# Kernel tuning notes

Hardware: AMD Instinct MI355X
Metric: run time of the kernel (lower is better)

Reference implementation:

```python
import jax, jax.numpy as jnp
from jax import lax
import numpy as np

C = 256       # residual_channels == skip_channels
B = 4
T = 4096
LATENT = 128
NB = 4        # n_blocks
NL = 10       # n_layers
ENC_DILS = tuple(2 ** i for i in range(NL)) * NB   # 40 encoder blocks
DEC_DILS = tuple(2 ** i for i in range(NL))        # 10 decoder blocks


def causal_conv(x, W, b, d):
    # x: [B, Cin, T], W: [Cout, Cin, k], left-pad by (k-1)*d for causality
    pad = (W.shape[-1] - 1) * d
    y = lax.conv_general_dilated(x, W, (1,), [(pad, 0)], rhs_dilation=(d,),
                                 dimension_numbers=('NCH', 'OIH', 'NCH'))
    return y + b[None, :, None]


def gated_block(h, Wf, bf, Wg, bg, Wr, br, Ws, bs, d):
    f = jnp.tanh(causal_conv(h, Wf, bf, d))
    g = jax.nn.sigmoid(causal_conv(h, Wg, bg, d))
    out = f * g
    res = jnp.einsum('oc,bct->bot', Wr, out) + br[None, :, None] + h
    skip = jnp.einsum('oc,bct->bot', Ws, out) + bs[None, :, None]
    return res, skip


def setup_inputs() -> dict:
    key = jax.random.key(0)
    ks = jax.random.split(key, 24)
    s = 0.05
    nE = NB * NL
    d = {}
    d['x'] = jax.random.normal(ks[0], (B, 1, T), jnp.float32)
    d['eps'] = jax.random.normal(ks[1], (B, LATENT), jnp.float32)
    d['enc_in_W'] = jax.random.normal(ks[2], (C, 1, 2)) * s
    d['enc_in_b'] = jnp.zeros((C,), jnp.float32)
    d['enc_Wf'] = jax.random.normal(ks[3], (nE, C, C, 2)) * s
    d['enc_bf'] = jnp.zeros((nE, C), jnp.float32)
    d['enc_Wg'] = jax.random.normal(ks[4], (nE, C, C, 2)) * s
    d['enc_bg'] = jnp.zeros((nE, C), jnp.float32)
    d['enc_Wr'] = jax.random.normal(ks[5], (nE, C, C)) * s
    d['enc_br'] = jnp.zeros((nE, C), jnp.float32)
    d['enc_Ws'] = jax.random.normal(ks[6], (nE, C, C)) * s
    d['enc_bs'] = jnp.zeros((nE, C), jnp.float32)
    d['fc_mu_W'] = jax.random.normal(ks[7], (LATENT, C)) * s
    d['fc_mu_b'] = jnp.zeros((LATENT,), jnp.float32)
    d['fc_lv_W'] = jax.random.normal(ks[8], (LATENT, C)) * s
    d['fc_lv_b'] = jnp.zeros((LATENT,), jnp.float32)
    d['dec_in_W'] = jax.random.normal(ks[9], (C, LATENT)) * s
    d['dec_in_b'] = jnp.zeros((C,), jnp.float32)
    d['dec_Wf'] = jax.random.normal(ks[10], (NL, C, C, 2)) * s
    d['dec_bf'] = jnp.zeros((NL, C), jnp.float32)
    d['dec_Wg'] = jax.random.normal(ks[11], (NL, C, C, 2)) * s
    d['dec_bg'] = jnp.zeros((NL, C), jnp.float32)
    d['dec_Wr'] = jax.random.normal(ks[12], (NL, C, C)) * s
    d['dec_br'] = jnp.zeros((NL, C), jnp.float32)
    d['out_W'] = jax.random.normal(ks[13], (1, C)) * s
    d['out_b'] = jnp.zeros((1,), jnp.float32)
    return d


def _forward(x, eps, enc_in_W, enc_in_b, enc_Wf, enc_bf, enc_Wg, enc_bg,
             enc_Wr, enc_br, enc_Ws, enc_bs, fc_mu_W, fc_mu_b, fc_lv_W, fc_lv_b,
             dec_in_W, dec_in_b, dec_Wf, dec_bf, dec_Wg, dec_bg, dec_Wr, dec_br,
             out_W, out_b):
    # --- encode ---
    h = causal_conv(x, enc_in_W, enc_in_b, 1)
    skip_sum = jnp.zeros((h.shape[0], C, h.shape[2]), h.dtype)
    for i, dil in enumerate(ENC_DILS):
        h, skip = gated_block(h, enc_Wf[i], enc_bf[i], enc_Wg[i], enc_bg[i],
                              enc_Wr[i], enc_br[i], enc_Ws[i], enc_bs[i], dil)
        skip_sum = skip_sum + skip
    pooled = skip_sum.mean(axis=-1)                      # [B, C]
    mu = pooled @ fc_mu_W.T + fc_mu_b                    # [B, LATENT]
    logvar = pooled @ fc_lv_W.T + fc_lv_b
    # --- reparameterize ---
    z = mu + eps * jnp.exp(0.5 * logvar)
    # --- decode (length-1 sequence) ---
    h2 = (jnp.einsum('ol,bl->bo', dec_in_W, z) + dec_in_b)[:, :, None]  # [B, C, 1]
    for i, dil in enumerate(DEC_DILS):
        f = jnp.tanh(causal_conv(h2, dec_Wf[i], dec_bf[i], dil))
        g = jax.nn.sigmoid(causal_conv(h2, dec_Wg[i], dec_bg[i], dil))
        out = f * g
        h2 = jnp.einsum('oc,bct->bot', dec_Wr[i], out) + dec_br[i][None, :, None] + h2
    y = jnp.einsum('oc,bct->bot', out_W, h2) + out_b[None, :, None]     # [B, 1, 1]
    return (y, mu, logvar)


def reference(x, eps, enc_in_W, enc_in_b, enc_Wf, enc_bf, enc_Wg, enc_bg,
              enc_Wr, enc_br, enc_Ws, enc_bs, fc_mu_W, fc_mu_b, fc_lv_W, fc_lv_b,
              dec_in_W, dec_in_b, dec_Wf, dec_bf, dec_Wg, dec_bg, dec_Wr, dec_br,
              out_W, out_b):
    return _forward(x, eps, enc_in_W, enc_in_b, enc_Wf, enc_bf, enc_Wg, enc_bg,
                    enc_Wr, enc_br, enc_Ws, enc_bs, fc_mu_W, fc_mu_b, fc_lv_W, fc_lv_b,
                    dec_in_W, dec_in_b, dec_Wf, dec_bf, dec_Wg, dec_bg, dec_Wr, dec_br,
                    out_W, out_b)
```

## Files before the change

### kernel.cpp

```cpp
#include <hip/hip_runtime.h>

typedef unsigned short u16;
typedef __attribute__((ext_vector_type(8))) __bf16 bf16x8;
typedef __attribute__((ext_vector_type(4))) float f32x4;

constexpr int C = 256;
constexpr int T = 4096;
constexpr int B = 4;
constexpr int NENC = 40;
constexpr int NDEC = 10;
constexpr int TILE = 64;

__device__ __forceinline__ float bf2f(u16 v) {
  union { unsigned u; float f; } x;
  x.u = ((unsigned)v) << 16;
  return x.f;
}
__device__ __forceinline__ u16 f2bf(float f) {
  union { float ff; unsigned u; } x;
  x.ff = f;
  unsigned r = x.u + 0x7fffu + ((x.u >> 16) & 1u);
  return (u16)(r >> 16);
}
__device__ __forceinline__ int swz(int row, int col) {
  int g = ((row & 7) ^ (row >> 3)) & 7;
  return row * 512 + (col ^ (g << 3));
}

typedef __attribute__((address_space(1))) const unsigned int* gp1_t;
typedef __attribute__((address_space(3))) unsigned int* lp3_t;
__device__ __forceinline__ void gl_lds16(const u16* g, u16* l) {
  __builtin_amdgcn_global_load_lds((gp1_t)(const void*)g, (lp3_t)(void*)l, 16, 0, 0);
}

__global__ void k_pack1(const float* __restrict__ Wf, const float* __restrict__ Wg,
                        u16* __restrict__ penc1, int total) {
  int p = blockIdx.x * 256 + threadIdx.x;
  if (p >= total) return;
  int lane = p & 63;
  int s = (p >> 6) & 3;
  int c = (p >> 8) & 15;
  int wv = (p >> 12) & 7;
  int layer = p >> 15;
  int co = wv * 32 + (s & 1) * 16 + (lane & 15);
  int k = c * 32 + (lane >> 4) * 8;
  const float* src = (s >= 2 ? Wg : Wf) + ((size_t)layer * C + co) * 512 + k;
  u16* dst = penc1 + (size_t)p * 8;
#pragma unroll
  for (int r = 0; r < 8; ++r) dst[r] = f2bf(src[r]);
}

__global__ void k_pack2(const float* __restrict__ Wr, u16* __restrict__ penc2, int total) {
  int p = blockIdx.x * 256 + threadIdx.x;
  if (p >= total) return;
  int lane = p & 63;
  int s = (p >> 6) & 1;
  int c = (p >> 7) & 7;
  int wv = (p >> 10) & 7;
  int layer = p >> 13;
  int co = wv * 32 + s * 16 + (lane & 15);
  int k = c * 32 + (lane >> 4) * 8;
  const float* src = Wr + ((size_t)layer * C + co) * 256 + k;
  u16* dst = penc2 + (size_t)p * 8;
#pragma unroll
  for (int r = 0; r < 8; ++r) dst[r] = f2bf(src[r]);
}

__global__ void k_packd(const float* __restrict__ dWf, const float* __restrict__ dWg,
                        const float* __restrict__ dWr, const float* __restrict__ dinW,
                        u16* __restrict__ pdfg, u16* __restrict__ pdr,
                        u16* __restrict__ tdin) {
  int p = blockIdx.x * 256 + threadIdx.x;
  if (p < 163840) {
    int lane = p & 63;
    int s = (p >> 6) & 1;
    int c = (p >> 7) & 7;
    int wv = (p >> 10) & 15;
    int layer = p >> 14;
    int co = wv * 16 + (lane & 15);
    int k = c * 32 + (lane >> 4) * 8;
    const float* src = (s ? dWg : dWf) + (((size_t)(layer * C + co)) * C + k) * 2 + 1;
    u16* dst = pdfg + (size_t)p * 8;
#pragma unroll
    for (int r = 0; r < 8; ++r) dst[r] = f2bf(src[2 * r]);
  } else if (p < 245760) {
    int q = p - 163840;
    int lane = q & 63;
    int c = (q >> 6) & 7;
    int wv = (q >> 9) & 15;
    int layer = q >> 13;
    int co = wv * 16 + (lane & 15);
    int k = c * 32 + (lane >> 4) * 8;
    const float* src = dWr + ((size_t)(layer * C + co)) * C + k;
    u16* dst = pdr + (size_t)q * 8;
#pragma unroll
    for (int r = 0; r < 8; ++r) dst[r] = f2bf(src[r]);
  } else if (p < 249856) {
    int u = p - 245760;
#pragma unroll
    for (int r = 0; r < 8; ++r) tdin[u * 8 + r] = f2bf(dinW[u * 8 + r]);
  }
}

__global__ void k_zero(float* __restrict__ p, int n) {
  int i = blockIdx.x * 256 + threadIdx.x;
  if (i < n) p[i] = 0.f;
}

__global__ void k_input(const float* __restrict__ x, const float* __restrict__ W,
                        const float* __restrict__ bin, float* __restrict__ h) {
  int idx = blockIdx.x * 256 + threadIdx.x;
  int t = idx & (T - 1);
  int c = (idx >> 12) & (C - 1);
  int b = idx >> 20;
  float xv = x[b * T + t];
  float xp = (t > 0) ? x[b * T + t - 1] : 0.f;
  h[idx] = W[2 * c] * xp + W[2 * c + 1] * xv + bin[c];
}

__global__ __launch_bounds__(512, 2) void k_enc(
    const float* __restrict__ hin, float* __restrict__ hout, float* __restrict__ rowsum_l,
    const u16* __restrict__ pw1, const float* __restrict__ bfb,
    const float* __restrict__ bgb,
    const u16* __restrict__ pw2, const float* __restrict__ brb,
    int dil) {
  extern __shared__ __align__(16) u16 smem[];
  u16* wb = smem + 64 * 512;
  const int tid = threadIdx.x;
  const int wave = tid >> 6;
  const int lane = tid & 63;
  const int ncol = lane & 15;
  const int quad = lane >> 4;
  const int wg = blockIdx.x;
  const int b = wg >> 6;
  const int t0 = (wg & 63) * TILE;
  const float* hb = hin + b * C * T;

  const int co0 = wave * 32;
  const int kq = quad * 8;
  const u16* b1 = pw1 + wave * 32768 + lane * 8;
  const u16* b2 = pw2 + wave * 8192 + lane * 8;
  const int aoff = lane * 8;

#pragma unroll
  for (int q = 0; q < 3; ++q) {
    u16* ld = wb + q * 16384 + wave * 2048;
    const u16* gs = b1 + q * 2048;
    gl_lds16(gs, ld);
    gl_lds16(gs + 512, ld + 512);
    gl_lds16(gs + 1024, ld + 1024);
    gl_lds16(gs + 1536, ld + 1536);
  }

  const int n4 = tid & 15;
  const int cib = tid >> 4;
  float4 v[16];
  const bool al4 = ((dil & 3) == 0);
  if (t0 >= dil) {
#pragma unroll
    for (int it2 = 0; it2 < 16; ++it2) {
      int ci = (cib + it2 * 32) & 255;
      int tap = it2 >> 3;
      int tb = t0 + n4 * 4 - (tap ? 0 : dil);
      const float* p = hb + ci * T + tb;
      if (tap || al4) {
        v[it2] = *(const float4*)p;
      } else {
        v[it2].x = p[0]; v[it2].y = p[1]; v[it2].z = p[2]; v[it2].w = p[3];
      }
    }
  } else {
#pragma unroll
    for (int it2 = 0; it2 < 16; ++it2) {
      int ci = (cib + it2 * 32) & 255;
      int tap = it2 >> 3;
      int tb = t0 + n4 * 4 - (tap ? 0 : dil);
      const float* p = hb + ci * T + tb;
      if (tap) {
        v[it2] = *(const float4*)p;
      } else {
        v[it2].x = (tb + 0 >= 0) ? p[0] : 0.f;
        v[it2].y = (tb + 1 >= 0) ? p[1] : 0.f;
        v[it2].z = (tb + 2 >= 0) ? p[2] : 0.f;
        v[it2].w = (tb + 3 >= 0) ? p[3] : 0.f;
      }
    }
  }
#pragma unroll
  for (int it2 = 0; it2 < 8; ++it2) {
    int ci = (cib + it2 * 32) & 255;
    const float* p0 = (const float*)&v[it2];
    const float* p1 = (const float*)&v[it2 + 8];
#pragma unroll
    for (int r = 0; r < 4; ++r) {
      unsigned w32 = (unsigned)f2bf(p0[r]) | ((unsigned)f2bf(p1[r]) << 16);
      *(unsigned*)(&smem[swz(n4 * 4 + r, 2 * ci)]) = w32;
    }
  }
  __syncthreads();

  f32x4 acc[4][4];
#pragma unroll
  for (int m = 0; m < 4; ++m)
#pragma unroll
    for (int nt = 0; nt < 4; ++nt)
      acc[m][nt] = (f32x4){0.f, 0.f, 0.f, 0.f};

#pragma unroll
  for (int c = 0; c < 16; ++c) {
    if (c <= 13)      asm volatile("s_waitcnt vmcnt(8)" ::: "memory");
    else if (c == 14) asm volatile("s_waitcnt vmcnt(4)" ::: "memory");
    else              asm volatile("s_waitcnt vmcnt(0)" ::: "memory");
    const u16* wr_ = wb + (c % 3) * 16384 + wave * 2048;
    bf16x8 af0 = *(const bf16x8*)(wr_ + aoff);
    bf16x8 af1 = *(const bf16x8*)(wr_ + 512 + aoff);
    bf16x8 af2 = *(const bf16x8*)(wr_ + 1024 + aoff);
    bf16x8 af3 = *(const bf16x8*)(wr_ + 1536 + aoff);
    const int kk = c * 32 + kq;
    bf16x8 bfr[4];
#pragma unroll
    for (int nt = 0; nt < 4; ++nt)
      bfr[nt] = *(const bf16x8*)(&smem[swz(nt * 16 + ncol, kk)]);
#pragma unroll
    for (int nt = 0; nt < 4; ++nt) {
      acc[0][nt] = __builtin_amdgcn_mfma_f32_16x16x32_bf16(af0, bfr[nt], acc[0][nt], 0, 0, 0);
      acc[1][nt] = __builtin_amdgcn_mfma_f32_16x16x32_bf16(af1, bfr[nt], acc[1][nt], 0, 0, 0);
      acc[2][nt] = __builtin_amdgcn_mfma_f32_16x16x32_bf16(af2, bfr[nt], acc[2][nt], 0, 0, 0);
      acc[3][nt] = __builtin_amdgcn_mfma_f32_16x16x32_bf16(af3, bfr[nt], acc[3][nt], 0, 0, 0);
    }
    if (c + 3 < 16) {
      asm volatile("s_waitcnt lgkmcnt(0)" ::: "memory");
      u16* ld = wb + (c % 3) * 16384 + wave * 2048;
      const u16* gs = b1 + (c + 3) * 2048;
      gl_lds16(gs, ld);
      gl_lds16(gs + 512, ld + 512);
      gl_lds16(gs + 1024, ld + 1024);
      gl_lds16(gs + 1536, ld + 1536);
    }
  }

#pragma unroll
  for (int q = 0; q < 3; ++q) {
    u16* ld = wb + q * 16384 + wave * 2048;
    const u16* gs = b2 + q * 1024;
    gl_lds16(gs, ld);
    gl_lds16(gs + 512, ld + 512);
  }
  __syncthreads();

  float* rsb = rowsum_l + b * C;
#pragma unroll
  for (int j = 0; j < 2; ++j) {
    const int cob = co0 + j * 16 + quad * 4;
    float bfv[4], bgv[4], rs[4];
#pragma unroll
    for (int r = 0; r < 4; ++r) {
      bfv[r] = bfb[cob + r];
      bgv[r] = bgb[cob + r];
      rs[r] = 0.f;
    }
#pragma unroll
    for (int nt = 0; nt < 4; ++nt) {
      const int n = nt * 16 + ncol;
      u16 pk[4];
#pragma unroll
      for (int r = 0; r < 4; ++r) {
        float fv = acc[j][nt][r] + bfv[r];
        float gv = acc[2 + j][nt][r] + bgv[r];
        float th = 1.f - 2.f / (__expf(2.f * fv) + 1.f);
        float sg = 1.f / (1.f + __expf(-gv));
        float o = th * sg;
        rs[r] += o;
        pk[r] = f2bf(o);
      }
      uint2 w;
      w.x = (unsigned)pk[0] | ((unsigned)pk[1] << 16);
      w.y = (unsigned)pk[2] | ((unsigned)pk[3] << 16);
      *(uint2*)(&smem[swz(n, cob)]) = w;
    }
#pragma unroll
    for (int r = 0; r < 4; ++r) {
      float s = rs[r];
      s += __shfl_xor(s, 1);
      s += __shfl_xor(s, 2);
      s += __shfl_xor(s, 4);
      s += __shfl_xor(s, 8);
      if (ncol == 0) atomicAdd(&rsb[cob + r], s);
    }
  }
  __syncthreads();

  f32x4 acc2[2][4];
#pragma unroll
  for (int m = 0; m < 2; ++m)
#pragma unroll
    for (int nt = 0; nt < 4; ++nt)
      acc2[m][nt] = (f32x4){0.f, 0.f, 0.f, 0.f};

#pragma unroll
  for (int c = 0; c < 8; ++c) {
    if (c <= 5)      asm volatile("s_waitcnt vmcnt(4)" ::: "memory");
    else if (c == 6) asm volatile("s_waitcnt vmcnt(2)" ::: "memory");
    else             asm volatile("s_waitcnt vmcnt(0)" ::: "memory");
    const u16* wr_ = wb + (c % 3) * 16384 + wave * 2048;
    bf16x8 af0 = *(const bf16x8*)(wr_ + aoff);
    bf16x8 af1 = *(const bf16x8*)(wr_ + 512 + aoff);
    const int kk = c * 32 + kq;
    bf16x8 bfr[4];
#pragma unroll
    for (int nt = 0; nt < 4; ++nt)
      bfr[nt] = *(const bf16x8*)(&smem[swz(nt * 16 + ncol, kk)]);
#pragma unroll
    for (int nt = 0; nt < 4; ++nt) {
      acc2[0][nt] = __builtin_amdgcn_mfma_f32_16x16x32_bf16(af0, bfr[nt], acc2[0][nt], 0, 0, 0);
      acc2[1][nt] = __builtin_amdgcn_mfma_f32_16x16x32_bf16(af1, bfr[nt], acc2[1][nt], 0, 0, 0);
    }
    if (c + 3 < 8) {
      asm volatile("s_waitcnt lgkmcnt(0)" ::: "memory");
      u16* ld = wb + (c % 3) * 16384 + wave * 2048;
      const u16* gs = b2 + (c + 3) * 1024;
      gl_lds16(gs, ld);
      gl_lds16(gs + 512, ld + 512);
    }
  }
  __syncthreads();

  float* fb = (float*)smem;
#pragma unroll
  for (int m = 0; m < 2; ++m) {
    const int cob = co0 + m * 16 + quad * 4;
#pragma unroll
    for (int nt = 0; nt < 4; ++nt) {
      const int t = nt * 16 + ncol;
#pragma unroll
      for (int r = 0; r < 4; ++r)
        fb[(cob + r) * 66 + t] = acc2[m][nt][r] + brb[cob + r];
    }
  }
  __syncthreads();
  float* ho = hout + b * C * T;
#pragma unroll
  for (int it2 = 0; it2 < 8; ++it2) {
    const int ci = cib + it2 * 32;
    const float* fr = fb + ci * 66 + n4 * 4;
    float4 o;
    o.x = fr[0] + v[it2 + 8].x;
    o.y = fr[1] + v[it2 + 8].y;
    o.z = fr[2] + v[it2 + 8].z;
    o.w = fr[3] + v[it2 + 8].w;
    *(float4*)(ho + ci * T + t0 + n4 * 4) = o;
  }
}

__global__ __launch_bounds__(256) void k_skip(
    const float* __restrict__ encWs, const float* __restrict__ encbs,
    const float* __restrict__ rowsum, float* __restrict__ pooled) {
  __shared__ float rs[B][C];
  const int l = blockIdx.x;
  const int co = threadIdx.x;
  for (int i = co; i < B * C; i += 256) rs[i >> 8][i & 255] = rowsum[l * B * C + i];
  __syncthreads();
  const float* Wrow = encWs + (size_t)l * C * C + co * C;
  float bs = encbs[l * C + co] * (float)T;
  float d[B] = {0.f, 0.f, 0.f, 0.f};
  for (int ci = 0; ci < C; ci += 4) {
    float4 w = *(const float4*)(Wrow + ci);
#pragma unroll
    for (int b = 0; b < B; ++b)
      d[b] += w.x * rs[b][ci] + w.y * rs[b][ci + 1] + w.z * rs[b][ci + 2] + w.w * rs[b][ci + 3];
  }
#pragma unroll
  for (int b = 0; b < B; ++b) atomicAdd(&pooled[b * C + co], d[b] + bs);
}

__global__ __launch_bounds__(256) void k_fc(
    const float* __restrict__ pooled,
    const float* __restrict__ muW, const float* __restrict__ mub,
    const float* __restrict__ lvW, const float* __restrict__ lvb,
    float* __restrict__ mlbuf, float* __restrict__ dout) {
  __shared__ float pm[B * C];
  const int tid = threadIdx.x;
  for (int i = tid; i < B * C; i += 256) pm[i] = pooled[i] * (1.f / (float)T);
  __syncthreads();
  const int waveG = blockIdx.x * 4 + (tid >> 6);
  const int lane = tid & 63;
  for (int j = 0; j < 16; ++j) {
    int d = waveG * 16 + j;
    int b = d >> 8, r = d & 255, which = r >> 7, l = r & 127;
    const float* Wrow = (which ? lvW : muW) + l * C;
    const float* p = pm + b * C;
    float s = Wrow[lane] * p[lane] + Wrow[lane + 64] * p[lane + 64] +
              Wrow[lane + 128] * p[lane + 128] + Wrow[lane + 192] * p[lane + 192];
#pragma unroll
    for (int off = 32; off; off >>= 1) s += __shfl_xor(s, off);
    if (lane == 0) {
      float val = s + (which ? lvb[l] : mub[l]);
      mlbuf[which * 512 + b * 128 + l] = val;
      dout[4 + which * 512 + b * 128 + l] = val;
    }
  }
}

__global__ __launch_bounds__(1024, 1) void k_dec(
    const float* __restrict__ mlbuf, const float* __restrict__ eps,
    const u16* __restrict__ tdin, const float* __restrict__ dinb,
    const u16* __restrict__ pdfg, const float* __restrict__ dbf,
    const float* __restrict__ dbg,
    const u16* __restrict__ pdr, const float* __restrict__ dbr,
    const float* __restrict__ outW, const float* __restrict__ outb,
    float* __restrict__ dout) {
  extern __shared__ __align__(16) u16 dsm[];
  __shared__ __align__(16) u16 Ah[16][264];
  __shared__ __align__(16) u16 Ao[16][264];
  __shared__ float h2f[4][256];
  __shared__ float outred[4];
  const int tid = threadIdx.x;
  const int wave = tid >> 6;
  const int lane = tid & 63;
  const int ncol = lane & 15;
  const int quad = lane >> 4;
  const int kq = quad * 8;
  const int co = wave * 16 + ncol;
  u16* wreg = dsm + wave * 4096;

  bf16x8 tdw[4];
  {
    const u16* wp = tdin + co * 128;
#pragma unroll
    for (int it = 0; it < 4; ++it) tdw[it] = *(const bf16x8*)(wp + it * 32 + kq);
  }

  if (tid < 512) {
    int b = tid >> 7, l = tid & 127;
    float mu = mlbuf[b * 128 + l];
    float lv = mlbuf[512 + b * 128 + l];
    Ah[b][l] = f2bf(mu + eps[b * 128 + l] * expf(0.5f * lv));
  }
  if (tid < 4) outred[tid] = 0.f;
  __syncthreads();

  {
    f32x4 acch = (f32x4){0.f, 0.f, 0.f, 0.f};
#pragma unroll
    for (int it = 0; it < 4; ++it) {
      bf16x8 af = *(const bf16x8*)(&Ah[ncol][it * 32 + kq]);
      acch = __builtin_amdgcn_mfma_f32_16x16x32_bf16(af, tdw[it], acch, 0, 0, 0);
    }
    __syncthreads();
    if (quad == 0) {
      float bias = dinb[co];
#pragma unroll
      for (int r = 0; r < 4; ++r) {
        float hv = acch[r] + bias;
        h2f[r][co] = hv;
        Ah[r][co] = f2bf(hv);
      }
    }
  }
  {
    const u16* fb = pdfg + wave * 8192 + lane * 8;
#pragma unroll
    for (int cc = 0; cc < 4; ++cc) {
      gl_lds16(fb + cc * 1024, wreg + cc * 1024);
      gl_lds16(fb + cc * 1024 + 512, wreg + cc * 1024 + 512);
    }
  }
  __syncthreads();

  for (int i = 0; i < NDEC; ++i) {
    const u16* fb = pdfg + (i * 16 + wave) * 8192 + lane * 8;
    const u16* rb = pdr + (i * 16 + wave) * 4096 + lane * 8;

    f32x4 accf = (f32x4){0.f, 0.f, 0.f, 0.f};
    f32x4 accg = (f32x4){0.f, 0.f, 0.f, 0.f};
#pragma unroll
    for (int c = 0; c < 8; ++c) {
      if (c == 4) asm volatile("s_waitcnt vmcnt(6)" ::: "memory");
      else if (c == 5) asm volatile("s_waitcnt vmcnt(4)" ::: "memory");
      else if (c == 6) asm volatile("s_waitcnt vmcnt(2)" ::: "memory");
      else if (c == 7) asm volatile("s_waitcnt vmcnt(0)" ::: "memory");
      const u16* bufp = wreg + (c & 3) * 1024;
      bf16x8 bf_ = *(const bf16x8*)(bufp + lane * 8);
      bf16x8 bg_ = *(const bf16x8*)(bufp + 512 + lane * 8);
      bf16x8 af = *(const bf16x8*)(&Ah[ncol][c * 32 + kq]);
      accf = __builtin_amdgcn_mfma_f32_16x16x32_bf16(af, bf_, accf, 0, 0, 0);
      accg = __builtin_amdgcn_mfma_f32_16x16x32_bf16(af, bg_, accg, 0, 0, 0);
      if (c < 4) {
        asm volatile("s_waitcnt lgkmcnt(0)" ::: "memory");
        gl_lds16(fb + (c + 4) * 1024, wreg + (c & 3) * 1024);
        gl_lds16(fb + (c + 4) * 1024 + 512, wreg + (c & 3) * 1024 + 512);
      }
    }
    asm volatile("s_waitcnt lgkmcnt(0)" ::: "memory");
#pragma unroll
    for (int cc = 0; cc < 4; ++cc) gl_lds16(rb + cc * 512, wreg + cc * 1024);

    if (quad == 0) {
      float bfv = dbf[i * C + co];
      float bgv = dbg[i * C + co];
#pragma unroll
      for (int r = 0; r < 4; ++r) {
        float fv = accf[r] + bfv;
        float gv = accg[r] + bgv;
        float th = 1.f - 2.f / (__expf(2.f * fv) + 1.f);
        float sg = 1.f / (1.f + __expf(-gv));
        Ao[r][co] = f2bf(th * sg);
      }
    }
    __syncthreads();

    f32x4 accr = (f32x4){0.f, 0.f, 0.f, 0.f};
#pragma unroll
    for (int c = 0; c < 8; ++c) {
      if (c == 4) asm volatile("s_waitcnt vmcnt(3)" ::: "memory");
      else if (c == 5) asm volatile("s_waitcnt vmcnt(2)" ::: "memory");
      else if (c == 6) asm volatile("s_waitcnt vmcnt(1)" ::: "memory");
      else if (c == 7) asm volatile("s_waitcnt vmcnt(0)" ::: "memory");
      bf16x8 br_ = *(const bf16x8*)(wreg + (c & 3) * 1024 + lane * 8);
      bf16x8 af = *(const bf16x8*)(&Ao[ncol][c * 32 + kq]);
      accr = __builtin_amdgcn_mfma_f32_16x16x32_bf16(af, br_, accr, 0, 0, 0);
      if (c < 4) {
        asm volatile("s_waitcnt lgkmcnt(0)" ::: "memory");
        gl_lds16(rb + (c + 4) * 512, wreg + (c & 3) * 1024);
      }
    }
    if (i + 1 < NDEC) {
      const u16* nfb = pdfg + ((i + 1) * 16 + wave) * 8192 + lane * 8;
      asm volatile("s_waitcnt lgkmcnt(0)" ::: "memory");
#pragma unroll
      for (int cc = 0; cc < 4; ++cc) {
        gl_lds16(nfb + cc * 1024, wreg + cc * 1024);
        gl_lds16(nfb + cc * 1024 + 512, wreg + cc * 1024 + 512);
      }
    }
    if (quad == 0) {
      float brv = dbr[i * C + co];
#pragma unroll
      for (int r = 0; r < 4; ++r) {
        float hv = h2f[r][co] + accr[r] + brv;
        h2f[r][co] = hv;
        Ah[r][co] = f2bf(hv);
      }
    }
    __syncthreads();
  }

  {
    int b = tid >> 8, c = tid & 255;
    float val = outW[c] * h2f[b][c];
#pragma unroll
    for (int off = 32; off; off >>= 1) val += __shfl_xor(val, off);
    if (lane == 0) atomicAdd(&outred[b], val);
  }
  __syncthreads();
  if (tid < 4) dout[tid] = outred[tid] + outb[0];
}

extern "C" void kernel_launch(void* const* d_in, const int* in_sizes, int n_in,
                              void* d_out, int out_size, void* d_ws, size_t ws_size,
                              hipStream_t stream) {
  const float* x      = (const float*)d_in[0];
  const float* eps    = (const float*)d_in[1];
  const float* encinW = (const float*)d_in[2];
  const float* encinb = (const float*)d_in[3];
  const float* encWf  = (const float*)d_in[4];
  const float* encbf  = (const float*)d_in[5];
  const float* encWg  = (const float*)d_in[6];
  const float* encbg  = (const float*)d_in[7];
  const float* encWr  = (const float*)d_in[8];
  const float* encbr  = (const float*)d_in[9];
  const float* encWs  = (const float*)d_in[10];
  const float* encbs  = (const float*)d_in[11];
  const float* muW    = (const float*)d_in[12];
  const float* mub    = (const float*)d_in[13];
  const float* lvW    = (const float*)d_in[14];
  const float* lvb    = (const float*)d_in[15];
  const float* dinW   = (const float*)d_in[16];
  const float* dinb   = (const float*)d_in[17];
  const float* dWf    = (const float*)d_in[18];
  const float* dbf    = (const float*)d_in[19];
  const float* dWg    = (const float*)d_in[20];
  const float* dbg    = (const float*)d_in[21];
  const float* dWr    = (const float*)d_in[22];
  const float* dbr    = (const float*)d_in[23];
  const float* outW   = (const float*)d_in[24];
  const float* outb   = (const float*)d_in[25];
  float* dout = (float*)d_out;

  char* ws = (char*)d_ws;
  float* hA = (float*)ws;
  float* hB = hA + (size_t)B * C * T;
  float* pooled = hB + (size_t)B * C * T;
  float* mlbuf = pooled + B * C;
  float* rowsum = mlbuf + 1024;
  u16* penc1 = (u16*)(rowsum + NENC * B * C);
  u16* penc2 = penc1 + (size_t)10485760;
  u16* pdfg = penc2 + (size_t)2621440;
  u16* pdr = pdfg + (size_t)1310720;
  u16* tdin = pdr + (size_t)655360;

  (void)hipFuncSetAttribute(reinterpret_cast<const void*>(k_enc),
                            hipFuncAttributeMaxDynamicSharedMemorySize, 163840);
  (void)hipFuncSetAttribute(reinterpret_cast<const void*>(k_dec),
                            hipFuncAttributeMaxDynamicSharedMemorySize, 131072);

  k_pack1<<<(1310720 + 255) / 256, 256, 0, stream>>>(encWf, encWg, penc1, 1310720);
  k_pack2<<<(327680 + 255) / 256, 256, 0, stream>>>(encWr, penc2, 327680);
  k_packd<<<(249856 + 255) / 256, 256, 0, stream>>>(dWf, dWg, dWr, dinW, pdfg, pdr, tdin);

  const int nZ = B * C + 1024 + NENC * B * C;
  k_zero<<<(nZ + 255) / 256, 256, 0, stream>>>(pooled, nZ);
  k_input<<<(B * C * T) / 256, 256, 0, stream>>>(x, encinW, encinb, hA);

  for (int i = 0; i < NENC; ++i) {
    const int dil = 1 << (i % 10);
    const float* hi = (i & 1) ? hB : hA;
    float* ho = (i & 1) ? hA : hB;
    k_enc<<<256, 512, 163840, stream>>>(
        hi, ho, rowsum + (size_t)i * B * C,
        penc1 + (size_t)i * 262144, encbf + (size_t)i * C,
        encbg + (size_t)i * C,
        penc2 + (size_t)i * 65536, encbr + (size_t)i * C,
        dil);
  }

  k_skip<<<NENC, 256, 0, stream>>>(encWs, encbs, rowsum, pooled);
  k_fc<<<16, 256, 0, stream>>>(pooled, muW, mub, lvW, lvb, mlbuf, dout);
  k_dec<<<1, 1024, 131072, stream>>>(mlbuf, eps, tdin, dinb, pdfg, dbf, dbg,
                                     pdr, dbr, outW, outb, dout);
}
```

Baseline: 1.321 ms.

## Halve encoder time tile to 32, shrink LDS, and split decoder into chained launches

The encoder kernel now processes 32 time steps per workgroup instead of 64, launching 512 workgroups with 64KB LDS instead of 256 with 160KB, and raises the launch-bounds occupancy target. The filter/gate weights are streamed through a double buffer in two passes (filter rows, then gate rows) rather than a triple buffer. The aim is more resident workgroups and fewer registers per thread, at the cost of loading the weights twice as often per output column. Separately, the single-block decoder is split into four launches that pass hidden state through a global buffer, which adds launch overhead and state round-trips for unclear benefit.

After: 1.802 ms. 36.4% more time.

```diff
diff --git a/kernel.cpp b/kernel.cpp
--- a/kernel.cpp
+++ b/kernel.cpp
@@ -9,7 +9,6 @@
 constexpr int B = 4;
 constexpr int NENC = 40;
 constexpr int NDEC = 10;
-constexpr int TILE = 64;
 
 __device__ __forceinline__ float bf2f(u16 v) {
   union { unsigned u; float f; } x;
@@ -118,130 +117,118 @@
   h[idx] = W[2 * c] * xp + W[2 * c + 1] * xv + bin[c];
 }
 
-__global__ __launch_bounds__(512, 2) void k_enc(
+__global__ __launch_bounds__(512, 4) void k_enc(
     const float* __restrict__ hin, float* __restrict__ hout, float* __restrict__ rowsum_l,
     const u16* __restrict__ pw1, const float* __restrict__ bfb,
     const float* __restrict__ bgb,
     const u16* __restrict__ pw2, const float* __restrict__ brb,
     int dil) {
   extern __shared__ __align__(16) u16 smem[];
-  u16* wb = smem + 64 * 512;
+  u16* wb = smem + 16384;
   const int tid = threadIdx.x;
   const int wave = tid >> 6;
   const int lane = tid & 63;
   const int ncol = lane & 15;
   const int quad = lane >> 4;
+  const int kq = quad * 8;
   const int wg = blockIdx.x;
-  const int b = wg >> 6;
-  const int t0 = (wg & 63) * TILE;
+  const int b = wg >> 7;
+  const int t0 = (wg & 127) * 32;
   const float* hb = hin + b * C * T;
 
   const int co0 = wave * 32;
-  const int kq = quad * 8;
   const u16* b1 = pw1 + wave * 32768 + lane * 8;
   const u16* b2 = pw2 + wave * 8192 + lane * 8;
+  u16* wbuf0 = wb + wave * 1024;
+  u16* wbuf1 = wb + 8192 + wave * 1024;
   const int aoff = lane * 8;
 
 #pragma unroll
-  for (int q = 0; q < 3; ++q) {
-    u16* ld = wb + q * 16384 + wave * 2048;
+  for (int q = 0; q < 2; ++q) {
+    u16* ld = q ? wbuf1 : wbuf0;
     const u16* gs = b1 + q * 2048;
     gl_lds16(gs, ld);
     gl_lds16(gs + 512, ld + 512);
-    gl_lds16(gs + 1024, ld + 1024);
-    gl_lds16(gs + 1536, ld + 1536);
-  }
-
-  const int n4 = tid & 15;
-  const int cib = tid >> 4;
-  float4 v[16];
+  }
+
+  const int n4 = tid & 7;
+  const int cib = tid >> 3;
+  float4 v[8];
   const bool al4 = ((dil & 3) == 0);
   if (t0 >= dil) {
 #pragma unroll
-    for (int it2 = 0; it2 < 16; ++it2) {
-      int ci = (cib + it2 * 32) & 255;
-      int tap = it2 >> 3;
-      int tb = t0 + n4 * 4 - (tap ? 0 : dil);
-      const float* p = hb + ci * T + tb;
-      if (tap || al4) {
-        v[it2] = *(const float4*)p;
-      } else {
-        v[it2].x = p[0]; v[it2].y = p[1]; v[it2].z = p[2]; v[it2].w = p[3];
-      }
+    for (int j = 0; j < 4; ++j) {
+      int ci = cib + j * 64;
+      const float* p0 = hb + ci * T + t0 + n4 * 4 - dil;
+      if (al4) v[j] = *(const float4*)p0;
+      else { v[j].x = p0[0]; v[j].y = p0[1]; v[j].z = p0[2]; v[j].w = p0[3]; }
+      v[4 + j] = *(const float4*)(hb + ci * T + t0 + n4 * 4);
     }
   } else {
 #pragma unroll
-    for (int it2 = 0; it2 < 16; ++it2) {
-      int ci = (cib + it2 * 32) & 255;
-      int tap = it2 >> 3;
-      int tb = t0 + n4 * 4 - (tap ? 0 : dil);
-      const float* p = hb + ci * T + tb;
-      if (tap) {
-        v[it2] = *(const float4*)p;
-      } else {
-        v[it2].x = (tb + 0 >= 0) ? p[0] : 0.f;
-        v[it2].y = (tb + 1 >= 0) ? p[1] : 0.f;
-        v[it2].z = (tb + 2 >= 0) ? p[2] : 0.f;
-        v[it2].w = (tb + 3 >= 0) ? p[3] : 0.f;
-      }
-    }
-  }
-#pragma unroll
-  for (int it2 = 0; it2 < 8; ++it2) {
-    int ci = (cib + it2 * 32) & 255;
-    const float* p0 = (const float*)&v[it2];
-    const float* p1 = (const float*)&v[it2 + 8];
+    for (int j = 0; j < 4; ++j) {
+      int ci = cib + j * 64;
+      int tb = t0 + n4 * 4 - dil;
+      const float* p0 = hb + ci * T + tb;
+      v[j].x = (tb + 0 >= 0) ? p0[0] : 0.f;
+      v[j].y = (tb + 1 >= 0) ? p0[1] : 0.f;
+      v[j].z = (tb + 2 >= 0) ? p0[2] : 0.f;
+      v[j].w = (tb + 3 >= 0) ? p0[3] : 0.f;
+      v[4 + j] = *(const float4*)(hb + ci * T + t0 + n4 * 4);
+    }
+  }
+#pragma unroll
+  for (int j = 0; j < 4; ++j) {
+    int ci = cib + j * 64;
+    const float* pa = (const float*)&v[j];
+    const float* pb = (const float*)&v[4 + j];
 #pragma unroll
     for (int r = 0; r < 4; ++r) {
-      unsigned w32 = (unsigned)f2bf(p0[r]) | ((unsigned)f2bf(p1[r]) << 16);
+      unsigned w32 = (unsigned)f2bf(pa[r]) | ((unsigned)f2bf(pb[r]) << 16);
       *(unsigned*)(&smem[swz(n4 * 4 + r, 2 * ci)]) = w32;
     }
   }
   __syncthreads();
 
-  f32x4 acc[4][4];
+  f32x4 acc[4][2];
 #pragma unroll
   for (int m = 0; m < 4; ++m)
 #pragma unroll
-    for (int nt = 0; nt < 4; ++nt)
+    for (int nt = 0; nt < 2; ++nt)
       acc[m][nt] = (f32x4){0.f, 0.f, 0.f, 0.f};
 
 #pragma unroll
-  for (int c = 0; c < 16; ++c) {
-    if (c <= 13)      asm volatile("s_waitcnt vmcnt(8)" ::: "memory");
-    else if (c == 14) asm volatile("s_waitcnt vmcnt(4)" ::: "memory");
-    else              asm volatile("s_waitcnt vmcnt(0)" ::: "memory");
-    const u16* wr_ = wb + (c % 3) * 16384 + wave * 2048;
-    bf16x8 af0 = *(const bf16x8*)(wr_ + aoff);
-    bf16x8 af1 = *(const bf16x8*)(wr_ + 512 + aoff);
-    bf16x8 af2 = *(const bf16x8*)(wr_ + 1024 + aoff);
-    bf16x8 af3 = *(const bf16x8*)(wr_ + 1536 + aoff);
+  for (int it = 0; it < 32; ++it) {
+    const int pass = it >> 4;
+    const int c = it & 15;
+    if (it < 31) asm volatile("s_waitcnt vmcnt(2)" ::: "memory");
+    else         asm volatile("s_waitcnt vmcnt(0)" ::: "memory");
+    const u16* wr_ = (it & 1) ? wbuf1 : wbuf0;
+    bf16x8 a0 = *(const bf16x8*)(wr_ + aoff);
+    bf16x8 a1 = *(const bf16x8*)(wr_ + 512 + aoff);
     const int kk = c * 32 + kq;
-    bf16x8 bfr[4];
-#pragma unroll
-    for (int nt = 0; nt < 4; ++nt)
+    bf16x8 bfr[2];
+#pragma unroll
+    for (int nt = 0; nt < 2; ++nt)
       bfr[nt] = *(const bf16x8*)(&smem[swz(nt * 16 + ncol, kk)]);
 #pragma unroll
-    for (int nt = 0; nt < 4; ++nt) {
-      acc[0][nt] = __builtin_amdgcn_mfma_f32_16x16x32_bf16(af0, bfr[nt], acc[0][nt], 0, 0, 0);
-      acc[1][nt] = __builtin_amdgcn_mfma_f32_16x16x32_bf16(af1, bfr[nt], acc[1][nt], 0, 0, 0);
-      acc[2][nt] = __builtin_amdgcn_mfma_f32_16x16x32_bf16(af2, bfr[nt], acc[2][nt], 0, 0, 0);
-      acc[3][nt] = __builtin_amdgcn_mfma_f32_16x16x32_bf16(af3, bfr[nt], acc[3][nt], 0, 0, 0);
-    }
-    if (c + 3 < 16) {
+    for (int nt = 0; nt < 2; ++nt) {
+      acc[pass * 2 + 0][nt] = __builtin_amdgcn_mfma_f32_16x16x32_bf16(a0, bfr[nt], acc[pass * 2 + 0][nt], 0, 0, 0);
+      acc[pass * 2 + 1][nt] = __builtin_amdgcn_mfma_f32_16x16x32_bf16(a1, bfr[nt], acc[pass * 2 + 1][nt], 0, 0, 0);
+    }
+    if (it + 2 < 32) {
       asm volatile("s_waitcnt lgkmcnt(0)" ::: "memory");
-      u16* ld = wb + (c % 3) * 16384 + wave * 2048;
-      const u16* gs = b1 + (c + 3) * 2048;
+      u16* ld = (it & 1) ? wbuf1 : wbuf0;
+      const int nit = it + 2;
+      const u16* gs = b1 + (nit & 15) * 2048 + ((nit >> 4) ? 1024 : 0);
       gl_lds16(gs, ld);
       gl_lds16(gs + 512, ld + 512);
-      gl_lds16(gs + 1024, ld + 1024);
-      gl_lds16(gs + 1536, ld + 1536);
-    }
-  }
-
-#pragma unroll
-  for (int q = 0; q < 3; ++q) {
-    u16* ld = wb + q * 16384 + wave * 2048;
+    }
+  }
+
+#pragma unroll
+  for (int q = 0; q < 2; ++q) {
+    u16* ld = q ? wbuf1 : wbuf0;
     const u16* gs = b2 + q * 1024;
     gl_lds16(gs, ld);
     gl_lds16(gs + 512, ld + 512);
@@ -260,8 +247,8 @@
       rs[r] = 0.f;
     }
 #pragma unroll
-    for (int nt = 0; nt < 4; ++nt) {
-      const int n = nt * 16 + ncol;
+    for (int nt = 0; nt < 2; ++nt) {
+      const int t = nt * 16 + ncol;
       u16 pk[4];
 #pragma unroll
       for (int r = 0; r < 4; ++r) {
@@ -276,7 +263,7 @@
       uint2 w;
       w.x = (unsigned)pk[0] | ((unsigned)pk[1] << 16);
       w.y = (unsigned)pk[2] | ((unsigned)pk[3] << 16);
-      *(uint2*)(&smem[swz(n, cob)]) = w;
+      *(uint2*)(&smem[swz(t, cob)]) = w;
     }
 #pragma unroll
     for (int r = 0; r < 4; ++r) {
@@ -290,35 +277,34 @@
   }
   __syncthreads();
 
-  f32x4 acc2[2][4];
+  f32x4 acc2[2][2];
 #pragma unroll
   for (int m = 0; m < 2; ++m)
 #pragma unroll
-    for (int nt = 0; nt < 4; ++nt)
+    for (int nt = 0; nt < 2; ++nt)
       acc2[m][nt] = (f32x4){0.f, 0.f, 0.f, 0.f};
 
 #pragma unroll
   for (int c = 0; c < 8; ++c) {
-    if (c <= 5)      asm volatile("s_waitcnt vmcnt(4)" ::: "memory");
-    else if (c == 6) asm volatile("s_waitcnt vmcnt(2)" ::: "memory");
-    else             asm volatile("s_waitcnt vmcnt(0)" ::: "memory");
-    const u16* wr_ = wb + (c % 3) * 16384 + wave * 2048;
-    bf16x8 af0 = *(const bf16x8*)(wr_ + aoff);
-    bf16x8 af1 = *(const bf16x8*)(wr_ + 512 + aoff);
+    if (c < 7) asm volatile("s_waitcnt vmcnt(2)" ::: "memory");
+    else       asm volatile("s_waitcnt vmcnt(0)" ::: "memory");
+    const u16* wr_ = (c & 1) ? wbuf1 : wbuf0;
+    bf16x8 a0 = *(const bf16x8*)(wr_ + aoff);
+    bf16x8 a1 = *(const bf16x8*)(wr_ + 512 + aoff);
     const int kk = c * 32 + kq;
-    bf16x8 bfr[4];
-#pragma unroll
-    for (int nt = 0; nt < 4; ++nt)
+    bf16x8 bfr[2];
+#pragma unroll
+    for (int nt = 0; nt < 2; ++nt)
       bfr[nt] = *(const bf16x8*)(&smem[swz(nt * 16 + ncol, kk)]);
 #pragma unroll
-    for (int nt = 0; nt < 4; ++nt) {
-      acc2[0][nt] = __builtin_amdgcn_mfma_f32_16x16x32_bf16(af0, bfr[nt], acc2[0][nt], 0, 0, 0);
-      acc2[1][nt] = __builtin_amdgcn_mfma_f32_16x16x32_bf16(af1, bfr[nt], acc2[1][nt], 0, 0, 0);
-    }
-    if (c + 3 < 8) {
+    for (int nt = 0; nt < 2; ++nt) {
+      acc2[0][nt] = __builtin_amdgcn_mfma_f32_16x16x32_bf16(a0, bfr[nt], acc2[0][nt], 0, 0, 0);
+      acc2[1][nt] = __builtin_amdgcn_mfma_f32_16x16x32_bf16(a1, bfr[nt], acc2[1][nt], 0, 0, 0);
+    }
+    if (c + 2 < 8) {
       asm volatile("s_waitcnt lgkmcnt(0)" ::: "memory");
-      u16* ld = wb + (c % 3) * 16384 + wave * 2048;
-      const u16* gs = b2 + (c + 3) * 1024;
+      u16* ld = (c & 1) ? wbuf1 : wbuf0;
+      const u16* gs = b2 + (c + 2) * 1024;
       gl_lds16(gs, ld);
       gl_lds16(gs + 512, ld + 512);
     }
@@ -330,24 +316,24 @@
   for (int m = 0; m < 2; ++m) {
     const int cob = co0 + m * 16 + quad * 4;
 #pragma unroll
-    for (int nt = 0; nt < 4; ++nt) {
+    for (int nt = 0; nt < 2; ++nt) {
       const int t = nt * 16 + ncol;
 #pragma unroll
       for (int r = 0; r < 4; ++r)
-        fb[(cob + r) * 66 + t] = acc2[m][nt][r] + brb[cob + r];
+        fb[(cob + r) * 34 + t] = acc2[m][nt][r] + brb[cob + r];
     }
   }
   __syncthreads();
   float* ho = hout + b * C * T;
 #pragma unroll
-  for (int it2 = 0; it2 < 8; ++it2) {
-    const int ci = cib + it2 * 32;
-    const float* fr = fb + ci * 66 + n4 * 4;
+  for (int j = 0; j < 4; ++j) {
+    const int ci = cib + j * 64;
+    const float* fr = fb + ci * 34 + n4 * 4;
     float4 o;
-    o.x = fr[0] + v[it2 + 8].x;
-    o.y = fr[1] + v[it2 + 8].y;
-    o.z = fr[2] + v[it2 + 8].z;
-    o.w = fr[3] + v[it2 + 8].w;
+    o.x = fr[0] + v[4 + j].x;
+    o.y = fr[1] + v[4 + j].y;
+    o.z = fr[2] + v[4 + j].z;
+    o.w = fr[3] + v[4 + j].w;
     *(float4*)(ho + ci * T + t0 + n4 * 4) = o;
   }
 }
@@ -408,7 +394,8 @@
     const float* __restrict__ dbg,
     const u16* __restrict__ pdr, const float* __restrict__ dbr,
     const float* __restrict__ outW, const float* __restrict__ outb,
-    float* __restrict__ dout) {
+    float* __restrict__ gstate, float* __restrict__ dout,
+    int l0, int l1, int head, int tail) {
   extern __shared__ __align__(16) u16 dsm[];
   __shared__ __align__(16) u16 Ah[16][264];
   __shared__ __align__(16) u16 Ao[16][264];
@@ -423,23 +410,20 @@
   const int co = wave * 16 + ncol;
   u16* wreg = dsm + wave * 4096;
 
-  bf16x8 tdw[4];
-  {
-    const u16* wp = tdin + co * 128;
-#pragma unroll
-    for (int it = 0; it < 4; ++it) tdw[it] = *(const bf16x8*)(wp + it * 32 + kq);
-  }
-
-  if (tid < 512) {
-    int b = tid >> 7, l = tid & 127;
-    float mu = mlbuf[b * 128 + l];
-    float lv = mlbuf[512 + b * 128 + l];
-    Ah[b][l] = f2bf(mu + eps[b * 128 + l] * expf(0.5f * lv));
-  }
-  if (tid < 4) outred[tid] = 0.f;
-  __syncthreads();
-
-  {
+  if (head) {
+    bf16x8 tdw[4];
+    {
+      const u16* wp = tdin + co * 128;
+#pragma unroll
+      for (int it = 0; it < 4; ++it) tdw[it] = *(const bf16x8*)(wp + it * 32 + kq);
+    }
+    if (tid < 512) {
+      int b = tid >> 7, l = tid & 127;
+      float mu = mlbuf[b * 128 + l];
+      float lv = mlbuf[512 + b * 128 + l];
+      Ah[b][l] = f2bf(mu + eps[b * 128 + l] * expf(0.5f * lv));
+    }
+    __syncthreads();
     f32x4 acch = (f32x4){0.f, 0.f, 0.f, 0.f};
 #pragma unroll
     for (int it = 0; it < 4; ++it) {
@@ -456,9 +440,15 @@
         Ah[r][co] = f2bf(hv);
       }
     }
-  }
+  } else {
+    float hv = gstate[tid & 1023];
+    int b = (tid >> 8) & 3, c = tid & 255;
+    h2f[b][c] = hv;
+    Ah[b][c] = f2bf(hv);
+  }
+  if (tid < 4) outred[tid] = 0.f;
   {
-    const u16* fb = pdfg + wave * 8192 + lane * 8;
+    const u16* fb = pdfg + (l0 * 16 + wave) * 8192 + lane * 8;
 #pragma unroll
     for (int cc = 0; cc < 4; ++cc) {
       gl_lds16(fb + cc * 1024, wreg + cc * 1024);
@@ -467,7 +457,7 @@
   }
   __syncthreads();
 
-  for (int i = 0; i < NDEC; ++i) {
+  for (int i = l0; i < l1; ++i) {
     const u16* fb = pdfg + (i * 16 + wave) * 8192 + lane * 8;
     const u16* rb = pdr + (i * 16 + wave) * 4096 + lane * 8;
 
@@ -524,7 +514,7 @@
         gl_lds16(rb + (c + 4) * 512, wreg + (c & 3) * 1024);
       }
     }
-    if (i + 1 < NDEC) {
+    if (i + 1 < l1) {
       const u16* nfb = pdfg + ((i + 1) * 16 + wave) * 8192 + lane * 8;
       asm volatile("s_waitcnt lgkmcnt(0)" ::: "memory");
 #pragma unroll
@@ -545,15 +535,17 @@
     __syncthreads();
   }
 
-  {
+  if (tail) {
     int b = tid >> 8, c = tid & 255;
     float val = outW[c] * h2f[b][c];
 #pragma unroll
     for (int off = 32; off; off >>= 1) val += __shfl_xor(val, off);
     if (lane == 0) atomicAdd(&outred[b], val);
-  }
-  __syncthreads();
-  if (tid < 4) dout[tid] = outred[tid] + outb[0];
+    __syncthreads();
+    if (tid < 4) dout[tid] = outred[tid] + outb[0];
+  } else {
+    gstate[tid & 1023] = h2f[(tid >> 8) & 3][tid & 255];
+  }
 }
 
 extern "C" void kernel_launch(void* const* d_in, const int* in_sizes, int n_in,
@@ -593,14 +585,15 @@
   float* pooled = hB + (size_t)B * C * T;
   float* mlbuf = pooled + B * C;
   float* rowsum = mlbuf + 1024;
-  u16* penc1 = (u16*)(rowsum + NENC * B * C);
+  float* gstate = rowsum + NENC * B * C;
+  u16* penc1 = (u16*)(gstate + 1024);
   u16* penc2 = penc1 + (size_t)10485760;
   u16* pdfg = penc2 + (size_t)2621440;
   u16* pdr = pdfg + (size_t)1310720;
   u16* tdin = pdr + (size_t)655360;
 
   (void)hipFuncSetAttribute(reinterpret_cast<const void*>(k_enc),
-                            hipFuncAttributeMaxDynamicSharedMemorySize, 163840);
+                            hipFuncAttributeMaxDynamicSharedMemorySize, 65536);
   (void)hipFuncSetAttribute(reinterpret_cast<const void*>(k_dec),
                             hipFuncAttributeMaxDynamicSharedMemorySize, 131072);
 
@@ -616,7 +609,7 @@
     const int dil = 1 << (i % 10);
     const float* hi = (i & 1) ? hB : hA;
     float* ho = (i & 1) ? hA : hB;
-    k_enc<<<256, 512, 163840, stream>>>(
+    k_enc<<<512, 512, 65536, stream>>>(
         hi, ho, rowsum + (size_t)i * B * C,
         penc1 + (size_t)i * 262144, encbf + (size_t)i * C,
         encbg + (size_t)i * C,
@@ -627,5 +620,11 @@
   k_skip<<<NENC, 256, 0, stream>>>(encWs, encbs, rowsum, pooled);
   k_fc<<<16, 256, 0, stream>>>(pooled, muW, mub, lvW, lvb, mlbuf, dout);
   k_dec<<<1, 1024, 131072, stream>>>(mlbuf, eps, tdin, dinb, pdfg, dbf, dbg,
-                                     pdr, dbr, outW, outb, dout);
-}
+                                     pdr, dbr, outW, outb, gstate, dout, 0, 3, 1, 0);
+  k_dec<<<1, 1024, 131072, stream>>>(mlbuf, eps, tdin, dinb, pdfg, dbf, dbg,
+                                     pdr, dbr, outW, outb, gstate, dout, 3, 6, 0, 0);
+  k_dec<<<1, 1024, 131072, stream>>>(mlbuf, eps, tdin, dinb, pdfg, dbf, dbg,
+                                     pdr, dbr, outW, outb, gstate, dout, 6, 8, 0, 0);
+  k_dec<<<1, 1024, 131072, stream>>>(mlbuf, eps, tdin, dinb, pdfg, dbf, dbg,
+                                     pdr, dbr, outW, outb, gstate, dout, 8, 10, 0, 1);
+}
```
